# Performance work log

Measured on AMD Instinct MI355X. Metric: run time of the kernel, lower is better.

Reference implementation:

```python
import jax, jax.numpy as jnp
import numpy as np

N, E = 100000, 1600000
IN_C, HID_C, OUT_C = 128, 256, 128


def _sage_conv(x, src, dst, Wl, Wr, b, n):
    # PyG SAGEConv (mean aggr): out_i = lin_l(mean_{j->i} x_j) + lin_r(x_i) + b
    msg = jax.ops.segment_sum(x[src], dst, num_segments=n)          # [N, F]
    deg = jax.ops.segment_sum(jnp.ones((src.shape[0],), x.dtype), dst, num_segments=n)
    mean = msg / jnp.maximum(deg, 1.0)[:, None]
    return mean @ Wl.T + x @ Wr.T + b


def setup_inputs() -> dict:
    key = jax.random.key(0)
    ks = jax.random.split(key, 9)
    x = jax.random.normal(ks[0], (N, IN_C), dtype=jnp.float32)
    edge_index = jax.random.randint(ks[1], (2, E), 0, N, dtype=jnp.int64)
    edge_attr = jax.random.normal(ks[2], (E, 1), dtype=jnp.float32)

    def glorot(k, fan_out, fan_in):
        s = np.sqrt(6.0 / (fan_in + fan_out)).astype(np.float32)
        return jax.random.uniform(k, (fan_out, fan_in), jnp.float32, -s, s)

    return {
        "x": x,
        "edge_index": edge_index,
        "edge_attr": edge_attr,
        "W1l": glorot(ks[3], HID_C, IN_C),
        "W1r": glorot(ks[4], HID_C, IN_C),
        "b1": jnp.zeros((HID_C,), jnp.float32),
        "W2l": glorot(ks[5], OUT_C, HID_C),
        "W2r": glorot(ks[6], OUT_C, HID_C),
        "b2": jnp.zeros((OUT_C,), jnp.float32),
    }


def reference(x, edge_index, edge_attr, W1l, W1r, b1, W2l, W2r, b2):
    src, dst = edge_index[0], edge_index[1]
    n = x.shape[0]
    h = _sage_conv(x, src, dst, W1l, W1r, b1, n)   # conv1
    h = jax.nn.relu(h)
    out = _sage_conv(h, src, dst, W2l, W2r, b2, n)  # conv2
    return out
```

## Files before the change

kernel.cpp:

```cpp
#include <hip/hip_runtime.h>


#define NBMAX 1024
#define BCAP  2560

using f32x4 = __attribute__((ext_vector_type(4))) float;
using s16x8 = __attribute__((ext_vector_type(8))) short;
using s16x2 = __attribute__((ext_vector_type(2))) short;

#define QSCALE 15.875f

__device__ inline unsigned short f2bf(float f) {
    unsigned int u = __float_as_uint(f);
    unsigned int r = u + 0x7fff + ((u >> 16) & 1);
    return (unsigned short)(r >> 16);
}
__device__ inline float bf2f(unsigned short b) {
    return __uint_as_float(((unsigned int)b) << 16);
}
__device__ inline float bflo(unsigned u) { return __uint_as_float(u << 16); }
__device__ inline float bfhi(unsigned u) { return __uint_as_float(u & 0xffff0000u); }

__global__ __launch_bounds__(256) void cursor_init_kernel(int* __restrict__ bcursor, int NB) {
    int i = blockIdx.x * 256 + threadIdx.x;
    if (i < NB) bcursor[i] = i * BCAP;
}

__global__ __launch_bounds__(1024) void bin_kernel(const int* __restrict__ srci,
                                                   const int* __restrict__ dsti,
                                                   int* __restrict__ bcursor,
                                                   unsigned* __restrict__ pairs, int E, int NB) {
    __shared__ int lh[NBMAX];
    __shared__ int lbase[NBMAX];
    for (int i = threadIdx.x; i < NB; i += 1024) lh[i] = 0;
    __syncthreads();
    int chunk = (E + gridDim.x - 1) / gridDim.x;
    int e0 = blockIdx.x * chunk;
    int e1 = min(e0 + chunk, E);
    for (int e = e0 + threadIdx.x; e < e1; e += 1024)
        atomicAdd(&lh[dsti[e] >> 7], 1);
    __syncthreads();
    for (int i = threadIdx.x; i < NB; i += 1024) {
        int c = lh[i];
        lbase[i] = c ? atomicAdd(&bcursor[i], c) : 0;
        lh[i] = 0;
    }
    __syncthreads();
    for (int e = e0 + threadIdx.x; e < e1; e += 1024) {
        int d = dsti[e];
        int bk = d >> 7;
        int pos = lbase[bk] + atomicAdd(&lh[bk], 1);
        pairs[pos] = ((unsigned)srci[e] << 7) | (unsigned)(d & 127);
    }
}

__global__ __launch_bounds__(256) void csr_build_kernel(const unsigned* __restrict__ pairs,
                                                        const int* __restrict__ bcursor,
                                                        int2* __restrict__ offs2,
                                                        int* __restrict__ csr, int n) {
    __shared__ int ldeg[128];
    __shared__ int s[128];
    __shared__ int lcur[128];
    int b = blockIdx.x, tid = threadIdx.x;
    int lo = b * BCAP, hi = bcursor[b];
    if (tid < 128) ldeg[tid] = 0;
    __syncthreads();
    for (int i = lo + tid; i < hi; i += 256)
        atomicAdd(&ldeg[pairs[i] & 127], 1);
    __syncthreads();
    if (tid < 128) s[tid] = ldeg[tid];
    __syncthreads();
    for (int d = 1; d < 128; d <<= 1) {
        int add = (tid < 128 && tid >= d) ? s[tid - d] : 0;
        __syncthreads();
        if (tid < 128) s[tid] += add;
        __syncthreads();
    }
    if (tid < 128) {
        int excl = lo + s[tid] - ldeg[tid];
        int node = b * 128 + tid;
        if (node < n) offs2[node] = make_int2(excl, excl + ldeg[tid]);
        lcur[tid] = excl;
    }
    __syncthreads();
    for (int i = lo + tid; i < hi; i += 256) {
        unsigned p = pairs[i];
        int pos = atomicAdd(&lcur[p & 127], 1);
        csr[pos] = (int)(p & ~127u);
    }
}

__global__ __launch_bounds__(256) void cvt_x_kernel(const float* __restrict__ x,
                                                    unsigned short* __restrict__ xb,
                                                    unsigned char* __restrict__ xq, int total4) {
    int i = blockIdx.x * 256 + threadIdx.x;
    int stride = gridDim.x * 256;
    for (; i < total4; i += stride) {
        float4 v = ((const float4*)x)[i];
        ushort4 o;
        o.x = f2bf(v.x); o.y = f2bf(v.y); o.z = f2bf(v.z); o.w = f2bf(v.w);
        ((ushort4*)xb)[i] = o;
        int q0 = max(-127, min(127, (int)rintf(v.x * QSCALE))) + 128;
        int q1 = max(-127, min(127, (int)rintf(v.y * QSCALE))) + 128;
        int q2 = max(-127, min(127, (int)rintf(v.z * QSCALE))) + 128;
        int q3 = max(-127, min(127, (int)rintf(v.w * QSCALE))) + 128;
        ((unsigned*)xq)[i] = (unsigned)q0 | ((unsigned)q1 << 8) |
                             ((unsigned)q2 << 16) | ((unsigned)q3 << 24);
    }
}

__global__ __launch_bounds__(256) void cvt_w_kernel(
    const float* __restrict__ W1l, const float* __restrict__ W1r,
    const float* __restrict__ W2l, const float* __restrict__ W2r,
    unsigned short* __restrict__ Wb1, unsigned short* __restrict__ Wb2l,
    unsigned short* __restrict__ Wb2r) {
    int idx = blockIdx.x * 256 + threadIdx.x;
    int which = idx >> 15;
    int r = idx & 32767;
    if (which == 0) {
        int o = r >> 7, k = r & 127;
        Wb1[o * 256 + k] = f2bf(W1l[r]);
    } else if (which == 1) {
        int o = r >> 7, k = r & 127;
        Wb1[o * 256 + 128 + k] = f2bf(W1r[r]);
    } else if (which == 2) {
        Wb2l[r] = f2bf(W2l[r]);
    } else {
        Wb2r[r] = f2bf(W2r[r]);
    }
}

template <bool OUT_F32>
__global__ __launch_bounds__(256) void agg_i8_kernel(const unsigned char* __restrict__ featq,
                                                     const int* __restrict__ csr,
                                                     const int2* __restrict__ offs2,
                                                     const unsigned short* __restrict__ uadd,
                                                     void* __restrict__ outp,
                                                     int n, int zoff, float dq) {
    int wave = threadIdx.x >> 6;
    int lane = threadIdx.x & 63;
    int node = blockIdx.x * 4 + wave;
    if (node >= n) return;
    int2 se = offs2[node];
    int start = se.x, end = se.y;
    int deg = end - start;
    int slot = lane >> 3;
    int c16 = lane & 7;

    s16x2 accE[4], accO[4];
#pragma unroll
    for (int j = 0; j < 4; ++j) { accE[j] = (s16x2){0, 0}; accO[j] = (s16x2){0, 0}; }

    auto addrow = [&](uint4 v) {
#pragma unroll
        for (int j = 0; j < 4; ++j) {
            unsigned u = (&v.x)[j];
            accE[j] += __builtin_bit_cast(s16x2, __builtin_amdgcn_perm(0u, u, 0x0C020C00u));
            accO[j] += __builtin_bit_cast(s16x2, __builtin_amdgcn_perm(0u, u, 0x0C030C01u));
        }
    };

    int nfull = deg >> 4;
    int e = start + slot;
    for (int it = 0; it < nfull; ++it, e += 16) {
        int o0 = csr[e];
        int o1 = csr[e + 8];
        uint4 v0 = *(const uint4*)(featq + (size_t)(unsigned)o0 + c16 * 16);
        uint4 v1 = *(const uint4*)(featq + (size_t)(unsigned)o1 + c16 * 16);
        addrow(v0);
        addrow(v1);
    }
    int done = start + (nfull << 4);
    int ntot = nfull << 4;
    if (done < end) {
        int se0 = done + slot;
        int se1 = done + 8 + slot;
        int o0 = (se0 < end) ? csr[se0] : zoff;
        int o1 = (se1 < end) ? csr[se1] : zoff;
        uint4 v0 = *(const uint4*)(featq + (size_t)(unsigned)o0 + c16 * 16);
        uint4 v1 = *(const uint4*)(featq + (size_t)(unsigned)o1 + c16 * 16);
        addrow(v0);
        addrow(v1);
        ntot += 16;
    }

#pragma unroll
    for (int m = 8; m <= 32; m <<= 1) {
#pragma unroll
        for (int j = 0; j < 4; ++j) {
            accE[j] += __builtin_bit_cast(s16x2, __shfl_xor(__builtin_bit_cast(int, accE[j]), m));
            accO[j] += __builtin_bit_cast(s16x2, __shfl_xor(__builtin_bit_cast(int, accO[j]), m));
        }
    }

    if (lane < 8) {
        float inv = dq / (float)max(deg, 1);
        float corr = 128.f * (float)ntot;
        if (OUT_F32) {
            const uint4* up = (const uint4*)(uadd + (size_t)node * 128 + c16 * 16);
            uint4 ua = up[0], ub = up[1];
            unsigned uw[8] = {ua.x, ua.y, ua.z, ua.w, ub.x, ub.y, ub.z, ub.w};
            float* dst = (float*)outp + (size_t)node * 128 + c16 * 16;
#pragma unroll
            for (int j = 0; j < 4; ++j) {
                float f0 = ((float)accE[j][0] - corr) * inv + bflo(uw[2 * j]);
                float f1 = ((float)accO[j][0] - corr) * inv + bfhi(uw[2 * j]);
                float f2 = ((float)accE[j][1] - corr) * inv + bflo(uw[2 * j + 1]);
                float f3 = ((float)accO[j][1] - corr) * inv + bfhi(uw[2 * j + 1]);
                *(float4*)(dst + 4 * j) = make_float4(f0, f1, f2, f3);
            }
        } else {
            unsigned wbuf[8];
#pragma unroll
            for (int j = 0; j < 4; ++j) {
                float f0 = ((float)accE[j][0] - corr) * inv;
                float f1 = ((float)accO[j][0] - corr) * inv;
                float f2 = ((float)accE[j][1] - corr) * inv;
                float f3 = ((float)accO[j][1] - corr) * inv;
                wbuf[2 * j]     = (unsigned)f2bf(f0) | ((unsigned)f2bf(f1) << 16);
                wbuf[2 * j + 1] = (unsigned)f2bf(f2) | ((unsigned)f2bf(f3) << 16);
            }
            uint4* dst = (uint4*)((unsigned short*)outp + (size_t)node * 128 + c16 * 16);
            dst[0] = make_uint4(wbuf[0], wbuf[1], wbuf[2], wbuf[3]);
            dst[1] = make_uint4(wbuf[4], wbuf[5], wbuf[6], wbuf[7]);
        }
    }
}

template <int OSTRIDE, int EPI>
__global__ __launch_bounds__(256) void gemm_persist_kernel(
    const unsigned short* __restrict__ A0, const unsigned short* __restrict__ A1,
    const unsigned short* __restrict__ Wb, const float* __restrict__ bias,
    void* __restrict__ outv, int n, int ntiles) {
    __shared__ unsigned short As[2][32 * 256];
    const int tid = threadIdx.x;
    const int w = tid >> 6, lane = tid & 63;
    const int l15 = lane & 15, lhi = lane >> 4;
    const int colbase = blockIdx.y * 128 + w * 32;

    s16x8 b[8][2];
#pragma unroll
    for (int kk = 0; kk < 8; ++kk)
#pragma unroll
        for (int cf = 0; cf < 2; ++cf)
            b[kk][cf] = *(const s16x8*)(Wb + (size_t)(colbase + cf * 16 + l15) * 256 +
                                        kk * 32 + lhi * 8);

    s16x8 st[4];
    auto stage_load = [&](int tile) {
#pragma unroll
        for (int p = 0; p < 4; ++p) {
            int chunk = p * 256 + tid;
            int row = chunk >> 5;
            int cc = chunk & 31;
            int grow = tile * 32 + row;
            if (grow >= n) grow = n - 1;
            const unsigned short* src;
            if (A1) {
                src = (cc < 16) ? (A0 + (size_t)grow * 128 + cc * 8)
                                : (A1 + (size_t)grow * 128 + (cc - 16) * 8);
            } else {
                src = A0 + (size_t)grow * 256 + cc * 8;
            }
            st[p] = *(const s16x8*)src;
        }
    };
    auto stage_write = [&](int buf) {
#pragma unroll
        for (int p = 0; p < 4; ++p) {
            int chunk = p * 256 + tid;
            int row = chunk >> 5;
            int cc = chunk & 31;
            int scc = (cc & 24) | ((cc ^ (row & 7)) & 7);
            *(s16x8*)((char*)&As[buf][0] + row * 512 + scc * 16) = st[p];
        }
    };

    int t = blockIdx.x;
    if (t >= ntiles) return;
    stage_load(t);
    stage_write(0);
    __syncthreads();
    int buf = 0;

    for (; t < ntiles; t += gridDim.x) {
        int tn = t + gridDim.x;
        bool hasNext = tn < ntiles;
        if (hasNext) stage_load(tn);

        f32x4 acc[2][2];
#pragma unroll
        for (int rf = 0; rf < 2; ++rf)
#pragma unroll
            for (int cf = 0; cf < 2; ++cf)
                acc[rf][cf] = (f32x4){0.f, 0.f, 0.f, 0.f};

#pragma unroll
        for (int kk = 0; kk < 8; ++kk) {
            s16x8 a[2];
#pragma unroll
            for (int rf = 0; rf < 2; ++rf) {
                int row = rf * 16 + l15;
                int cbase = kk * 4 + lhi;
                int scc = (cbase & 24) | ((cbase ^ (row & 7)) & 7);
                a[rf] = *(const s16x8*)((const char*)&As[buf][0] + row * 512 + scc * 16);
            }
#pragma unroll
            for (int rf = 0; rf < 2; ++rf)
#pragma unroll
                for (int cf = 0; cf < 2; ++cf)
                    acc[rf][cf] = __builtin_amdgcn_mfma_f32_16x16x32_bf16(
                        b[kk][cf], a[rf], acc[rf][cf], 0, 0, 0);
        }

        __syncthreads();
        if (hasNext) stage_write(buf ^ 1);
        __syncthreads();

#pragma unroll
        for (int rf = 0; rf < 2; ++rf) {
            int row = t * 32 + rf * 16 + l15;
            if (row >= n) continue;
#pragma unroll
            for (int cf = 0; cf < 2; ++cf) {
                int colg = colbase + cf * 16 + lhi * 4;
                f32x4 v = acc[rf][cf];
                float4 bb = *(const float4*)(bias + colg);
                v[0] += bb.x; v[1] += bb.y; v[2] += bb.z; v[3] += bb.w;
                if (EPI == 1) {
                    v[0] = fmaxf(v[0], 0.f); v[1] = fmaxf(v[1], 0.f);
                    v[2] = fmaxf(v[2], 0.f); v[3] = fmaxf(v[3], 0.f);
                }
                uint2 o;
                o.x = (unsigned)f2bf(v[0]) | ((unsigned)f2bf(v[1]) << 16);
                o.y = (unsigned)f2bf(v[2]) | ((unsigned)f2bf(v[3]) << 16);
                *(uint2*)((unsigned short*)outv + (size_t)row * OSTRIDE + colg) = o;
            }
        }
        buf ^= 1;
    }
}

__global__ __launch_bounds__(256, 2) void gemm_dual_kernel(
    const unsigned short* __restrict__ A0,
    const unsigned short* __restrict__ WbL, const unsigned short* __restrict__ WbR,
    const float* __restrict__ bias,
    unsigned char* __restrict__ tq, unsigned short* __restrict__ u,
    int n, int ntiles) {
    __shared__ unsigned short As[2][32 * 256];
    const int tid = threadIdx.x;
    const int w = tid >> 6, lane = tid & 63;
    const int l15 = lane & 15, lhi = lane >> 4;
    const int colbase = w * 32;

    s16x8 bL[8][2], bR[8][2];
#pragma unroll
    for (int kk = 0; kk < 8; ++kk)
#pragma unroll
        for (int cf = 0; cf < 2; ++cf) {
            size_t off = (size_t)(colbase + cf * 16 + l15) * 256 + kk * 32 + lhi * 8;
            bL[kk][cf] = *(const s16x8*)(WbL + off);
            bR[kk][cf] = *(const s16x8*)(WbR + off);
        }

    s16x8 st[4];
    auto stage_load = [&](int tile) {
#pragma unroll
        for (int p = 0; p < 4; ++p) {
            int chunk = p * 256 + tid;
            int row = chunk >> 5;
            int cc = chunk & 31;
            int grow = tile * 32 + row;
            if (grow >= n) grow = n - 1;
            st[p] = *(const s16x8*)(A0 + (size_t)grow * 256 + cc * 8);
        }
    };
    auto stage_write = [&](int buf) {
#pragma unroll
        for (int p = 0; p < 4; ++p) {
            int chunk = p * 256 + tid;
            int row = chunk >> 5;
            int cc = chunk & 31;
            int scc = (cc & 24) | ((cc ^ (row & 7)) & 7);
            *(s16x8*)((char*)&As[buf][0] + row * 512 + scc * 16) = st[p];
        }
    };

    int t = blockIdx.x;
    if (t >= ntiles) return;
    stage_load(t);
    stage_write(0);
    __syncthreads();
    int buf = 0;

    for (; t < ntiles; t += gridDim.x) {
        int tn = t + gridDim.x;
        bool hasNext = tn < ntiles;
        if (hasNext) stage_load(tn);

        f32x4 accL[2][2], accR[2][2];
#pragma unroll
        for (int rf = 0; rf < 2; ++rf)
#pragma unroll
            for (int cf = 0; cf < 2; ++cf) {
                accL[rf][cf] = (f32x4){0.f, 0.f, 0.f, 0.f};
                accR[rf][cf] = (f32x4){0.f, 0.f, 0.f, 0.f};
            }

#pragma unroll
        for (int kk = 0; kk < 8; ++kk) {
            s16x8 a[2];
#pragma unroll
            for (int rf = 0; rf < 2; ++rf) {
                int row = rf * 16 + l15;
                int cbase = kk * 4 + lhi;
                int scc = (cbase & 24) | ((cbase ^ (row & 7)) & 7);
                a[rf] = *(const s16x8*)((const char*)&As[buf][0] + row * 512 + scc * 16);
            }
#pragma unroll
            for (int rf = 0; rf < 2; ++rf)
#pragma unroll
                for (int cf = 0; cf < 2; ++cf) {
                    accL[rf][cf] = __builtin_amdgcn_mfma_f32_16x16x32_bf16(
                        bL[kk][cf], a[rf], accL[rf][cf], 0, 0, 0);
                    accR[rf][cf] = __builtin_amdgcn_mfma_f32_16x16x32_bf16(
                        bR[kk][cf], a[rf], accR[rf][cf], 0, 0, 0);
                }
        }

        __syncthreads();
        if (hasNext) stage_write(buf ^ 1);
        __syncthreads();

#pragma unroll
        for (int rf = 0; rf < 2; ++rf) {
            int row = t * 32 + rf * 16 + l15;
            if (row >= n) continue;
#pragma unroll
            for (int cf = 0; cf < 2; ++cf) {
                int colg = colbase + cf * 16 + lhi * 4;
                f32x4 vL = accL[rf][cf];
                int q0 = max(-127, min(127, (int)rintf(vL[0] * QSCALE))) + 128;
                int q1 = max(-127, min(127, (int)rintf(vL[1] * QSCALE))) + 128;
                int q2 = max(-127, min(127, (int)rintf(vL[2] * QSCALE))) + 128;
                int q3 = max(-127, min(127, (int)rintf(vL[3] * QSCALE))) + 128;
                unsigned oq = (unsigned)q0 | ((unsigned)q1 << 8) |
                              ((unsigned)q2 << 16) | ((unsigned)q3 << 24);
                *(unsigned*)(tq + (size_t)row * 128 + colg) = oq;
                f32x4 vR = accR[rf][cf];
                float4 bb = *(const float4*)(bias + colg);
                vR[0] += bb.x; vR[1] += bb.y; vR[2] += bb.z; vR[3] += bb.w;
                uint2 ou;
                ou.x = (unsigned)f2bf(vR[0]) | ((unsigned)f2bf(vR[1]) << 16);
                ou.y = (unsigned)f2bf(vR[2]) | ((unsigned)f2bf(vR[3]) << 16);
                *(uint2*)(u + (size_t)row * 128 + colg) = ou;
            }
        }
        buf ^= 1;
    }
}

extern "C" void kernel_launch(void* const* d_in, const int* in_sizes, int n_in,
                              void* d_out, int out_size, void* d_ws, size_t ws_size,
                              hipStream_t stream) {
    const float* x   = (const float*)d_in[0];
    const int*   ei  = (const int*)d_in[1];
    const float* W1l = (const float*)d_in[3];
    const float* W1r = (const float*)d_in[4];
    const float* b1  = (const float*)d_in[5];
    const float* W2l = (const float*)d_in[6];
    const float* W2r = (const float*)d_in[7];
    const float* b2  = (const float*)d_in[8];

    const int n = in_sizes[0] / 128;
    const int E = in_sizes[1] / 2;
    const int* srci = ei;
    const int* dsti = ei + E;
    const int NB = (n + 127) >> 7;

    char* w = (char*)d_ws;
    auto alloc = [&](size_t bytes) {
        char* p = w;
        w += (bytes + 255) & ~(size_t)255;
        return p;
    };
    int*      bcursor = (int*)alloc((size_t)NBMAX * 4);
    int2*     offs2   = (int2*)alloc((size_t)n * 8);
    unsigned* pairs   = (unsigned*)alloc((size_t)NB * BCAP * 4);
    int*      csr     = (int*)alloc((size_t)NB * BCAP * 4);
    unsigned short* Wb1   = (unsigned short*)alloc((size_t)256 * 256 * 2);
    unsigned short* Wb2l  = (unsigned short*)alloc((size_t)128 * 256 * 2);
    unsigned short* Wb2r  = (unsigned short*)alloc((size_t)128 * 256 * 2);
    unsigned short* xb    = (unsigned short*)alloc((size_t)n * 128 * 2);
    unsigned char*  xq    = (unsigned char*)alloc((size_t)(n + 1) * 128);
    unsigned short* mean1b= (unsigned short*)alloc((size_t)n * 128 * 2);
    unsigned short* hb    = (unsigned short*)alloc((size_t)n * 256 * 2);
    unsigned char*  tq    = (unsigned char*)alloc((size_t)(n + 1) * 128);
    float*          outp  = (float*)d_out;

    cursor_init_kernel<<<(NB + 255) / 256, 256, 0, stream>>>(bcursor, NB);
    bin_kernel<<<256, 1024, 0, stream>>>(srci, dsti, bcursor, pairs, E, NB);
    csr_build_kernel<<<NB, 256, 0, stream>>>(pairs, bcursor, offs2, csr, n);

    hipMemsetAsync(xq + (size_t)n * 128, 0x80, 128, stream);
    hipMemsetAsync(tq + (size_t)n * 128, 0x80, 128, stream);
    cvt_x_kernel<<<2048, 256, 0, stream>>>(x, xb, xq, n * 128 / 4);
    cvt_w_kernel<<<(4 * 32768) / 256, 256, 0, stream>>>(W1l, W1r, W2l, W2r, Wb1, Wb2l, Wb2r);

    const int ntiles = (n + 31) / 32;
    const int zoff = n * 128;
    const float dq = 1.f / QSCALE;
    agg_i8_kernel<false><<<(n + 3) / 4, 256, 0, stream>>>(xq, csr, offs2, nullptr, mean1b, n, zoff, dq);
    gemm_persist_kernel<256, 1><<<dim3(768, 2), 256, 0, stream>>>(mean1b, xb, Wb1, b1, hb, n, ntiles);
    gemm_dual_kernel<<<512, 256, 0, stream>>>(hb, Wb2l, Wb2r, b2, tq, mean1b, n, ntiles);
    agg_i8_kernel<true><<<(n + 3) / 4, 256, 0, stream>>>(tq, csr, offs2, mean1b, outp, n, zoff, dq);
}
```

Before: 222.4 us.

## Merge init and conversion kernels, use nontemporal accesses, persistent-grid aggregation

Folds the cursor init and the two sentinel-row memsets into one tiny init kernel, and merges the weight conversion into the x conversion kernel, removing three launches. The x conversion and the aggregation epilogue now use nontemporal loads and stores. Both aggregation kernels switch from one block per 4 nodes to a grid-stride loop over 2048 blocks. Risks are that nontemporal stores bypass the cache for data the next kernel reads, and that the persistent grid balances degree-skewed nodes less well.

Result: faster. 217.0 us (-2.4%).

```diff
diff --git a/kernel.cpp b/kernel.cpp
--- a/kernel.cpp
+++ b/kernel.cpp
@@ -5,6 +5,8 @@
 #define BCAP  2560
 
 using f32x4 = __attribute__((ext_vector_type(4))) float;
+using u32x4 = __attribute__((ext_vector_type(4))) unsigned;
+using u16x4 = __attribute__((ext_vector_type(4))) unsigned short;
 using s16x8 = __attribute__((ext_vector_type(8))) short;
 using s16x2 = __attribute__((ext_vector_type(2))) short;
 
@@ -15,15 +17,16 @@
     unsigned int r = u + 0x7fff + ((u >> 16) & 1);
     return (unsigned short)(r >> 16);
 }
-__device__ inline float bf2f(unsigned short b) {
-    return __uint_as_float(((unsigned int)b) << 16);
-}
 __device__ inline float bflo(unsigned u) { return __uint_as_float(u << 16); }
 __device__ inline float bfhi(unsigned u) { return __uint_as_float(u & 0xffff0000u); }
 
-__global__ __launch_bounds__(256) void cursor_init_kernel(int* __restrict__ bcursor, int NB) {
-    int i = blockIdx.x * 256 + threadIdx.x;
-    if (i < NB) bcursor[i] = i * BCAP;
+__global__ __launch_bounds__(1024) void init_kernel(int* __restrict__ bcursor,
+                                                    unsigned* __restrict__ xqz,
+                                                    unsigned* __restrict__ tqz, int NB) {
+    int t = threadIdx.x;
+    if (t < NB) bcursor[t] = t * BCAP;
+    if (t < 32) xqz[t] = 0x80808080u;
+    else if (t < 64) tqz[t - 32] = 0x80808080u;
 }
 
 __global__ __launch_bounds__(1024) void bin_kernel(const int* __restrict__ srci,
@@ -90,43 +93,48 @@
     }
 }
 
-__global__ __launch_bounds__(256) void cvt_x_kernel(const float* __restrict__ x,
-                                                    unsigned short* __restrict__ xb,
-                                                    unsigned char* __restrict__ xq, int total4) {
+__global__ __launch_bounds__(256) void cvt_kernel(const float* __restrict__ x,
+                                                  unsigned short* __restrict__ xb,
+                                                  unsigned char* __restrict__ xq, int total4,
+                                                  const float* __restrict__ W1l,
+                                                  const float* __restrict__ W1r,
+                                                  const float* __restrict__ W2l,
+                                                  const float* __restrict__ W2r,
+                                                  unsigned short* __restrict__ Wb1,
+                                                  unsigned short* __restrict__ Wb2l,
+                                                  unsigned short* __restrict__ Wb2r) {
+    if (blockIdx.x < 128) {
+        for (int k = threadIdx.x; k < 1024; k += 256) {
+            int idx = blockIdx.x * 1024 + k;
+            int which = idx >> 15;
+            int r = idx & 32767;
+            if (which == 0) {
+                int o = r >> 7, kk = r & 127;
+                Wb1[o * 256 + kk] = f2bf(W1l[r]);
+            } else if (which == 1) {
+                int o = r >> 7, kk = r & 127;
+                Wb1[o * 256 + 128 + kk] = f2bf(W1r[r]);
+            } else if (which == 2) {
+                Wb2l[r] = f2bf(W2l[r]);
+            } else {
+                Wb2r[r] = f2bf(W2r[r]);
+            }
+        }
+    }
     int i = blockIdx.x * 256 + threadIdx.x;
     int stride = gridDim.x * 256;
     for (; i < total4; i += stride) {
-        float4 v = ((const float4*)x)[i];
-        ushort4 o;
+        f32x4 v = __builtin_nontemporal_load((const f32x4*)x + i);
+        u16x4 o;
         o.x = f2bf(v.x); o.y = f2bf(v.y); o.z = f2bf(v.z); o.w = f2bf(v.w);
-        ((ushort4*)xb)[i] = o;
+        __builtin_nontemporal_store(o, (u16x4*)xb + i);
         int q0 = max(-127, min(127, (int)rintf(v.x * QSCALE))) + 128;
         int q1 = max(-127, min(127, (int)rintf(v.y * QSCALE))) + 128;
         int q2 = max(-127, min(127, (int)rintf(v.z * QSCALE))) + 128;
         int q3 = max(-127, min(127, (int)rintf(v.w * QSCALE))) + 128;
-        ((unsigned*)xq)[i] = (unsigned)q0 | ((unsigned)q1 << 8) |
-                             ((unsigned)q2 << 16) | ((unsigned)q3 << 24);
-    }
-}
-
-__global__ __launch_bounds__(256) void cvt_w_kernel(
-    const float* __restrict__ W1l, const float* __restrict__ W1r,
-    const float* __restrict__ W2l, const float* __restrict__ W2r,
-    unsigned short* __restrict__ Wb1, unsigned short* __restrict__ Wb2l,
-    unsigned short* __restrict__ Wb2r) {
-    int idx = blockIdx.x * 256 + threadIdx.x;
-    int which = idx >> 15;
-    int r = idx & 32767;
-    if (which == 0) {
-        int o = r >> 7, k = r & 127;
-        Wb1[o * 256 + k] = f2bf(W1l[r]);
-    } else if (which == 1) {
-        int o = r >> 7, k = r & 127;
-        Wb1[o * 256 + 128 + k] = f2bf(W1r[r]);
-    } else if (which == 2) {
-        Wb2l[r] = f2bf(W2l[r]);
-    } else {
-        Wb2r[r] = f2bf(W2r[r]);
+        unsigned qo = (unsigned)q0 | ((unsigned)q1 << 8) |
+                      ((unsigned)q2 << 16) | ((unsigned)q3 << 24);
+        __builtin_nontemporal_store(qo, (unsigned*)xq + i);
     }
 }
 
@@ -139,90 +147,97 @@
                                                      int n, int zoff, float dq) {
     int wave = threadIdx.x >> 6;
     int lane = threadIdx.x & 63;
-    int node = blockIdx.x * 4 + wave;
-    if (node >= n) return;
-    int2 se = offs2[node];
-    int start = se.x, end = se.y;
-    int deg = end - start;
     int slot = lane >> 3;
     int c16 = lane & 7;
 
-    s16x2 accE[4], accO[4];
-#pragma unroll
-    for (int j = 0; j < 4; ++j) { accE[j] = (s16x2){0, 0}; accO[j] = (s16x2){0, 0}; }
-
-    auto addrow = [&](uint4 v) {
-#pragma unroll
-        for (int j = 0; j < 4; ++j) {
-            unsigned u = (&v.x)[j];
-            accE[j] += __builtin_bit_cast(s16x2, __builtin_amdgcn_perm(0u, u, 0x0C020C00u));
-            accO[j] += __builtin_bit_cast(s16x2, __builtin_amdgcn_perm(0u, u, 0x0C030C01u));
-        }
-    };
-
-    int nfull = deg >> 4;
-    int e = start + slot;
-    for (int it = 0; it < nfull; ++it, e += 16) {
-        int o0 = csr[e];
-        int o1 = csr[e + 8];
-        uint4 v0 = *(const uint4*)(featq + (size_t)(unsigned)o0 + c16 * 16);
-        uint4 v1 = *(const uint4*)(featq + (size_t)(unsigned)o1 + c16 * 16);
-        addrow(v0);
-        addrow(v1);
-    }
-    int done = start + (nfull << 4);
-    int ntot = nfull << 4;
-    if (done < end) {
-        int se0 = done + slot;
-        int se1 = done + 8 + slot;
-        int o0 = (se0 < end) ? csr[se0] : zoff;
-        int o1 = (se1 < end) ? csr[se1] : zoff;
-        uint4 v0 = *(const uint4*)(featq + (size_t)(unsigned)o0 + c16 * 16);
-        uint4 v1 = *(const uint4*)(featq + (size_t)(unsigned)o1 + c16 * 16);
-        addrow(v0);
-        addrow(v1);
-        ntot += 16;
-    }
-
-#pragma unroll
-    for (int m = 8; m <= 32; m <<= 1) {
-#pragma unroll
-        for (int j = 0; j < 4; ++j) {
-            accE[j] += __builtin_bit_cast(s16x2, __shfl_xor(__builtin_bit_cast(int, accE[j]), m));
-            accO[j] += __builtin_bit_cast(s16x2, __shfl_xor(__builtin_bit_cast(int, accO[j]), m));
-        }
-    }
-
-    if (lane < 8) {
-        float inv = dq / (float)max(deg, 1);
-        float corr = 128.f * (float)ntot;
-        if (OUT_F32) {
-            const uint4* up = (const uint4*)(uadd + (size_t)node * 128 + c16 * 16);
-            uint4 ua = up[0], ub = up[1];
-            unsigned uw[8] = {ua.x, ua.y, ua.z, ua.w, ub.x, ub.y, ub.z, ub.w};
-            float* dst = (float*)outp + (size_t)node * 128 + c16 * 16;
+    for (int base = blockIdx.x * 4; base < n; base += gridDim.x * 4) {
+        int node = base + wave;
+        if (node >= n) continue;
+        int2 se = offs2[node];
+        int start = se.x, end = se.y;
+        int deg = end - start;
+
+        s16x2 accE[4], accO[4];
+#pragma unroll
+        for (int j = 0; j < 4; ++j) { accE[j] = (s16x2){0, 0}; accO[j] = (s16x2){0, 0}; }
+
+        auto addrow = [&](u32x4 v) {
 #pragma unroll
             for (int j = 0; j < 4; ++j) {
-                float f0 = ((float)accE[j][0] - corr) * inv + bflo(uw[2 * j]);
-                float f1 = ((float)accO[j][0] - corr) * inv + bfhi(uw[2 * j]);
-                float f2 = ((float)accE[j][1] - corr) * inv + bflo(uw[2 * j + 1]);
-                float f3 = ((float)accO[j][1] - corr) * inv + bfhi(uw[2 * j + 1]);
-                *(float4*)(dst + 4 * j) = make_float4(f0, f1, f2, f3);
-            }
-        } else {
-            unsigned wbuf[8];
+                unsigned u = v[j];
+                accE[j] += __builtin_bit_cast(s16x2, __builtin_amdgcn_perm(0u, u, 0x0C020C00u));
+                accO[j] += __builtin_bit_cast(s16x2, __builtin_amdgcn_perm(0u, u, 0x0C030C01u));
+            }
+        };
+
+        int nfull = deg >> 4;
+        int e = start + slot;
+        for (int it = 0; it < nfull; ++it, e += 16) {
+            int o0 = csr[e];
+            int o1 = csr[e + 8];
+            u32x4 v0 = *(const u32x4*)(featq + (size_t)(unsigned)o0 + c16 * 16);
+            u32x4 v1 = *(const u32x4*)(featq + (size_t)(unsigned)o1 + c16 * 16);
+            addrow(v0);
+            addrow(v1);
+        }
+        int done = start + (nfull << 4);
+        int ntot = nfull << 4;
+        if (done < end) {
+            int se0 = done + slot;
+            int se1 = done + 8 + slot;
+            int o0 = (se0 < end) ? csr[se0] : zoff;
+            int o1 = (se1 < end) ? csr[se1] : zoff;
+            u32x4 v0 = *(const u32x4*)(featq + (size_t)(unsigned)o0 + c16 * 16);
+            u32x4 v1 = *(const u32x4*)(featq + (size_t)(unsigned)o1 + c16 * 16);
+            addrow(v0);
+            addrow(v1);
+            ntot += 16;
+        }
+
+#pragma unroll
+        for (int m = 8; m <= 32; m <<= 1) {
 #pragma unroll
             for (int j = 0; j < 4; ++j) {
-                float f0 = ((float)accE[j][0] - corr) * inv;
-                float f1 = ((float)accO[j][0] - corr) * inv;
-                float f2 = ((float)accE[j][1] - corr) * inv;
-                float f3 = ((float)accO[j][1] - corr) * inv;
-                wbuf[2 * j]     = (unsigned)f2bf(f0) | ((unsigned)f2bf(f1) << 16);
-                wbuf[2 * j + 1] = (unsigned)f2bf(f2) | ((unsigned)f2bf(f3) << 16);
-            }
-            uint4* dst = (uint4*)((unsigned short*)outp + (size_t)node * 128 + c16 * 16);
-            dst[0] = make_uint4(wbuf[0], wbuf[1], wbuf[2], wbuf[3]);
-            dst[1] = make_uint4(wbuf[4], wbuf[5], wbuf[6], wbuf[7]);
+                accE[j] += __builtin_bit_cast(s16x2, __shfl_xor(__builtin_bit_cast(int, accE[j]), m));
+                accO[j] += __builtin_bit_cast(s16x2, __shfl_xor(__builtin_bit_cast(int, accO[j]), m));
+            }
+        }
+
+        if (lane < 8) {
+            float inv = dq / (float)max(deg, 1);
+            float corr = 128.f * (float)ntot;
+            if (OUT_F32) {
+                const u32x4* up = (const u32x4*)(uadd + (size_t)node * 128 + c16 * 16);
+                u32x4 ua = __builtin_nontemporal_load(up);
+                u32x4 ub = __builtin_nontemporal_load(up + 1);
+                unsigned uw[8] = {ua.x, ua.y, ua.z, ua.w, ub.x, ub.y, ub.z, ub.w};
+                float* dst = (float*)outp + (size_t)node * 128 + c16 * 16;
+#pragma unroll
+                for (int j = 0; j < 4; ++j) {
+                    f32x4 fv;
+                    fv[0] = ((float)accE[j][0] - corr) * inv + bflo(uw[2 * j]);
+                    fv[1] = ((float)accO[j][0] - corr) * inv + bfhi(uw[2 * j]);
+                    fv[2] = ((float)accE[j][1] - corr) * inv + bflo(uw[2 * j + 1]);
+                    fv[3] = ((float)accO[j][1] - corr) * inv + bfhi(uw[2 * j + 1]);
+                    __builtin_nontemporal_store(fv, (f32x4*)(dst + 4 * j));
+                }
+            } else {
+                unsigned wbuf[8];
+#pragma unroll
+                for (int j = 0; j < 4; ++j) {
+                    float f0 = ((float)accE[j][0] - corr) * inv;
+                    float f1 = ((float)accO[j][0] - corr) * inv;
+                    float f2 = ((float)accE[j][1] - corr) * inv;
+                    float f3 = ((float)accO[j][1] - corr) * inv;
+                    wbuf[2 * j]     = (unsigned)f2bf(f0) | ((unsigned)f2bf(f1) << 16);
+                    wbuf[2 * j + 1] = (unsigned)f2bf(f2) | ((unsigned)f2bf(f3) << 16);
+                }
+                u32x4* dst = (u32x4*)((unsigned short*)outp + (size_t)node * 128 + c16 * 16);
+                u32x4 w0 = {wbuf[0], wbuf[1], wbuf[2], wbuf[3]};
+                u32x4 w1 = {wbuf[4], wbuf[5], wbuf[6], wbuf[7]};
+                __builtin_nontemporal_store(w0, dst);
+                __builtin_nontemporal_store(w1, dst + 1);
+            }
         }
     }
 }
@@ -498,20 +513,18 @@
     unsigned char*  tq    = (unsigned char*)alloc((size_t)(n + 1) * 128);
     float*          outp  = (float*)d_out;
 
-    cursor_init_kernel<<<(NB + 255) / 256, 256, 0, stream>>>(bcursor, NB);
+    init_kernel<<<1, 1024, 0, stream>>>(bcursor, (unsigned*)(xq + (size_t)n * 128),
+                                        (unsigned*)(tq + (size_t)n * 128), NB);
     bin_kernel<<<256, 1024, 0, stream>>>(srci, dsti, bcursor, pairs, E, NB);
     csr_build_kernel<<<NB, 256, 0, stream>>>(pairs, bcursor, offs2, csr, n);
-
-    hipMemsetAsync(xq + (size_t)n * 128, 0x80, 128, stream);
-    hipMemsetAsync(tq + (size_t)n * 128, 0x80, 128, stream);
-    cvt_x_kernel<<<2048, 256, 0, stream>>>(x, xb, xq, n * 128 / 4);
-    cvt_w_kernel<<<(4 * 32768) / 256, 256, 0, stream>>>(W1l, W1r, W2l, W2r, Wb1, Wb2l, Wb2r);
+    cvt_kernel<<<2048, 256, 0, stream>>>(x, xb, xq, n * 128 / 4,
+                                         W1l, W1r, W2l, W2r, Wb1, Wb2l, Wb2r);
 
     const int ntiles = (n + 31) / 32;
     const int zoff = n * 128;
     const float dq = 1.f / QSCALE;
-    agg_i8_kernel<false><<<(n + 3) / 4, 256, 0, stream>>>(xq, csr, offs2, nullptr, mean1b, n, zoff, dq);
+    agg_i8_kernel<false><<<2048, 256, 0, stream>>>(xq, csr, offs2, nullptr, mean1b, n, zoff, dq);
     gemm_persist_kernel<256, 1><<<dim3(768, 2), 256, 0, stream>>>(mean1b, xb, Wb1, b1, hb, n, ntiles);
     gemm_dual_kernel<<<512, 256, 0, stream>>>(hb, Wb2l, Wb2r, b2, tq, mean1b, n, ntiles);
-    agg_i8_kernel<true><<<(n + 3) / 4, 256, 0, stream>>>(tq, csr, offs2, mean1b, outp, n, zoff, dq);
-}
+    agg_i8_kernel<true><<<2048, 256, 0, stream>>>(tq, csr, offs2, mean1b, outp, n, zoff, dq);
+}
```
